# Kernel optimization log

Measured on AMD Instinct MI355X. Metric: run time of the kernel, lower is better.

The kernel has to match this reference:

```python
import jax, jax.numpy as jnp
import numpy as np

NTOKENS = 50257
NHID = 1024
TPC = int(np.ceil(np.sqrt(NTOKENS)))          # 225 tokens per class
NCLASSES = int(np.ceil(NTOKENS / TPC))        # 224 classes
BATCH = 2048
INITRANGE = 0.1


def setup_inputs() -> dict:
    key = jax.random.key(0)
    k1, k2, k3, k4 = jax.random.split(key, 4)
    inputs = jax.random.normal(k1, (BATCH, NHID), dtype=jnp.float32)
    labels = jax.random.randint(k2, (BATCH,), 0, NTOKENS, dtype=jnp.int32)
    W_top = jax.random.uniform(k3, (NHID, NCLASSES), dtype=jnp.float32,
                               minval=-INITRANGE, maxval=INITRANGE)
    b_top = jnp.zeros((NCLASSES,), dtype=jnp.float32)
    W_bottom = jax.random.uniform(k4, (NCLASSES, NHID, TPC), dtype=jnp.float32,
                                  minval=-INITRANGE, maxval=INITRANGE)
    b_bottom = jnp.zeros((NCLASSES, TPC), dtype=jnp.float32)
    return {"inputs": inputs, "labels": labels, "W_top": W_top, "b_top": b_top,
            "W_bottom": W_bottom, "b_bottom": b_bottom}


def reference(inputs, labels, W_top, b_top, W_bottom, b_bottom):
    # Two-level hierarchical softmax: P(word) = P(class | h) * P(word | class, h)
    batch = inputs.shape[0]
    cls = labels // TPC          # [B] class index at top level
    word = labels % TPC          # [B] word index within class

    # Top level: [B, nclasses]
    top_probs = jax.nn.softmax(inputs @ W_top + b_top, axis=1)
    p_cls = top_probs[jnp.arange(batch), cls]            # [B]

    # Bottom level: gather per-example class weights then batched matvec
    Wb = W_bottom[cls]                                    # [B, nhid, tpc]
    bb = b_bottom[cls]                                    # [B, tpc]
    bottom_logits = jnp.einsum('bd,bdk->bk', inputs, Wb) + bb
    bottom_probs = jax.nn.softmax(bottom_logits, axis=1)
    p_word = bottom_probs[jnp.arange(batch), word]        # [B]

    return p_cls * p_word
```

## Files before the change

kernel.cpp:

```cpp
#include <hip/hip_runtime.h>
#include <math.h>

#define TPC 225
#define NCLS 224
#define NHID 1024
#define BATCH 2048
#define CAP 256
#define LSTRIDE 256
#define NCHUNK 8
#define CHUNK_D 128
#define NDQ 32

__global__ __launch_bounds__(256) void hs_bucket(const int* __restrict__ labels,
                                                 int* __restrict__ bucket,
                                                 int* __restrict__ cnt) {
    __shared__ int scnt[NCLS];
    const int t = threadIdx.x;
    for (int i = t; i < NCLS; i += 256) scnt[i] = 0;
    __syncthreads();
    for (int b = t; b < BATCH; b += 256) {
        int lab = labels[b];
        int c = lab / TPC;
        int pos = atomicAdd(&scnt[c], 1);
        bucket[c * CAP + pos] = b;
    }
    __syncthreads();
    for (int i = t; i < NCLS; i += 256) cnt[i] = scnt[i];
}

#define LOADW(W)                                              \
    do {                                                      \
        _Pragma("unroll") for (int di = 0; di < 4; di++)      \
            _Pragma("unroll") for (int j = 0; j < 4; j++)     \
                W[di][j] = pj[j][di * KS];                    \
        _Pragma("unroll") for (int j = 0; j < 4; j++)         \
            pj[j] += 4 * KS;                                  \
    } while (0)

#define LOADX(X, dq)                                          \
    do {                                                      \
        _Pragma("unroll") for (int rl = 0; rl < RW; rl++)     \
            X[rl] = *(const float4*)(xp[rl] + (dq) * 4);      \
    } while (0)

#define FMAS(W, X)                                            \
    do {                                                      \
        _Pragma("unroll") for (int rl = 0; rl < RW; rl++) {   \
            _Pragma("unroll") for (int di = 0; di < 4; di++) {\
                float xv = ((const float*)&X[rl])[di];        \
                _Pragma("unroll") for (int j = 0; j < 4; j++) \
                    acc[rl][j] = fmaf(xv, W[di][j], acc[rl][j]); \
            }                                                 \
        }                                                     \
    } while (0)

template <int RW, int KS>
__device__ __forceinline__ void gemm_chunk(const float* __restrict__ xb,
                                           const int* rows,
                                           const float* __restrict__ wq,
                                           const int lane,
                                           float acc[RW][4]) {
    const float* xp[RW];
#pragma unroll
    for (int rl = 0; rl < RW; rl++) xp[rl] = xb + (size_t)rows[rl] * NHID;
    const float* pj[4];
#pragma unroll
    for (int j = 0; j < 4; j++) {
        int k = 64 * j + lane;
        pj[j] = wq + (k < KS ? k : KS - 1);
    }
#pragma unroll
    for (int rl = 0; rl < RW; rl++)
#pragma unroll
        for (int j = 0; j < 4; j++) acc[rl][j] = 0.f;

    float wA[4][4], wB[4][4];
    float4 xA[RW], xB[RW];
    LOADW(wA);
    LOADX(xA, 0);
    for (int dq = 0; dq < NDQ; dq += 2) {
        LOADW(wB);
        LOADX(xB, dq + 1);
        FMAS(wA, xA);
        if (dq + 2 < NDQ) {
            LOADW(wA);
            LOADX(xA, dq + 2);
        }
        FMAS(wB, xB);
    }
}

__global__ __launch_bounds__(256, 4) void hs_tlogits(const float* __restrict__ x,
                                                     const float* __restrict__ W,
                                                     float* __restrict__ twsP) {
    const int rb = blockIdx.x >> 3;
    const int q = blockIdx.x & 7;
    const int lane = threadIdx.x & 63;
    const int wr = threadIdx.x >> 6;
    int rows[2] = {rb * 8 + wr * 2, rb * 8 + wr * 2 + 1};
    const float* xb = x + q * CHUNK_D;
    const float* wq = W + (size_t)q * CHUNK_D * NCLS;
    float acc[2][4];
    gemm_chunk<2, NCLS>(xb, rows, wq, lane, acc);
    float* tp = twsP + (size_t)q * BATCH * LSTRIDE;
#pragma unroll
    for (int rl = 0; rl < 2; rl++)
#pragma unroll
        for (int j = 0; j < 4; j++) {
            int k = 64 * j + lane;
            if (k < NCLS) tp[(size_t)rows[rl] * LSTRIDE + k] = acc[rl][j];
        }
}

template <int RW>
__device__ __forceinline__ void bchunk(const float* __restrict__ xb,
                                       const float* __restrict__ wq,
                                       const int* __restrict__ bucket_c,
                                       const int base, const int n,
                                       const int lane, const int wr,
                                       float* __restrict__ bp) {
    int rows[RW], rval[RW];
#pragma unroll
    for (int rl = 0; rl < RW; rl++) {
        int idx = base + wr * RW + rl;
        rows[rl] = bucket_c[idx < n ? idx : 0];
        rval[rl] = (idx < n);
    }
    float acc[RW][4];
    gemm_chunk<RW, TPC>(xb, rows, wq, lane, acc);
#pragma unroll
    for (int rl = 0; rl < RW; rl++) {
        if (rval[rl]) {
#pragma unroll
            for (int j = 0; j < 4; j++) {
                int k = 64 * j + lane;
                if (k < TPC) bp[(size_t)rows[rl] * LSTRIDE + k] = acc[rl][j];
            }
        }
    }
}

__global__ __launch_bounds__(256, 4) void hs_blogits(const float* __restrict__ x,
                                                     const float* __restrict__ Wb,
                                                     const int* __restrict__ bucket,
                                                     const int* __restrict__ cnt,
                                                     float* __restrict__ bws) {
    const int c = blockIdx.x >> 3;
    const int q = blockIdx.x & 7;
    const int n = cnt[c];
    if (n == 0) return;
    const int lane = threadIdx.x & 63;
    const int wr = threadIdx.x >> 6;
    const float* wq = Wb + (size_t)c * (NHID * TPC) + (size_t)q * CHUNK_D * TPC;
    const float* xb = x + q * CHUNK_D;
    const int* bucket_c = bucket + c * CAP;
    float* bp = bws + (size_t)q * BATCH * LSTRIDE;

    for (int base = 0; base < n; base += 16) {
        int m = n - base;
        if (m > 16) m = 16;
        const int RW = (m + 3) >> 2;
        switch (RW) {
            case 1: bchunk<1>(xb, wq, bucket_c, base, n, lane, wr, bp); break;
            case 2: bchunk<2>(xb, wq, bucket_c, base, n, lane, wr, bp); break;
            case 3: bchunk<3>(xb, wq, bucket_c, base, n, lane, wr, bp); break;
            default: bchunk<4>(xb, wq, bucket_c, base, n, lane, wr, bp); break;
        }
    }
}

__global__ __launch_bounds__(256) void hs_finish(const float* __restrict__ tws,
                                                 const float* __restrict__ bws,
                                                 const int* __restrict__ labels,
                                                 const float* __restrict__ b_top,
                                                 const float* __restrict__ b_bot,
                                                 float* __restrict__ out) {
    const int lane = threadIdx.x & 63;
    const int wave = threadIdx.x >> 6;
    const int row = blockIdx.x * 4 + wave;
    const int label = labels[row];
    const int c = label / TPC;
    const int word = label - c * TPC;

    float p[2];
#pragma unroll
    for (int lvl = 0; lvl < 2; lvl++) {
        const int NS = lvl ? TPC : NCLS;
        const int pick = lvl ? word : c;
        const float* lws = lvl ? bws : tws;
        const float* bias = lvl ? (b_bot + c * TPC) : b_top;
        float lg[4];
#pragma unroll
        for (int j = 0; j < 4; j++) {
            int k = lane + 64 * j;
            if (k < NS) {
                float v = 0.f;
#pragma unroll
                for (int pq = 0; pq < NCHUNK; pq++)
                    v += lws[((size_t)pq * BATCH + row) * LSTRIDE + k];
                lg[j] = v + bias[k];
            } else {
                lg[j] = -INFINITY;
            }
        }
        float m = fmaxf(fmaxf(lg[0], lg[1]), fmaxf(lg[2], lg[3]));
#pragma unroll
        for (int off = 32; off > 0; off >>= 1) m = fmaxf(m, __shfl_xor(m, off, 64));
        float s = 0.f, pp = 0.f;
#pragma unroll
        for (int j = 0; j < 4; j++) {
            int k = lane + 64 * j;
            float e = (k < NS) ? __expf(lg[j] - m) : 0.f;
            s += e;
            if (k == pick) pp = e;
        }
#pragma unroll
        for (int off = 32; off > 0; off >>= 1) {
            s += __shfl_xor(s, off, 64);
            pp += __shfl_xor(pp, off, 64);
        }
        p[lvl] = pp / s;
    }
    if (lane == 0) out[row] = p[0] * p[1];
}

extern "C" void kernel_launch(void* const* d_in, const int* in_sizes, int n_in,
                              void* d_out, int out_size, void* d_ws, size_t ws_size,
                              hipStream_t stream) {
    const float* inputs   = (const float*)d_in[0];
    const int*   labels   = (const int*)d_in[1];
    const float* W_top    = (const float*)d_in[2];
    const float* b_top    = (const float*)d_in[3];
    const float* W_bottom = (const float*)d_in[4];
    const float* b_bottom = (const float*)d_in[5];
    float* out = (float*)d_out;

    int* bucket = (int*)d_ws;
    int* cnt    = bucket + NCLS * CAP;
    float* tws  = (float*)(cnt + NCLS);
    float* bws  = tws + (size_t)NCHUNK * BATCH * LSTRIDE;

    hs_bucket<<<1, 256, 0, stream>>>(labels, bucket, cnt);
    hs_tlogits<<<256 * NCHUNK, 256, 0, stream>>>(inputs, W_top, tws);
    hs_blogits<<<NCLS * NCHUNK, 256, 0, stream>>>(inputs, W_bottom, bucket, cnt, bws);
    hs_finish<<<BATCH / 4, 256, 0, stream>>>(tws, bws, labels, b_top, b_bottom, out);
}
```

Baseline: 409.9 us.

## Stage weight slabs into LDS with async double-buffered global_load_lds

Both logit GEMMs now copy 16-row weight slabs into shared memory with the direct global-to-LDS load builtin, double-buffered so the next slab loads while the current one is used. Each lane reads float4 weight vectors from LDS and owns four contiguous output columns, which allows vectorized float4 stores. The aim is to cut per-lane global weight load latency and instruction count in the inner loop. In exchange it adds a block-wide barrier per slab and LDS use that may lower occupancy, and the bottom kernel restages the weights on every 16-row pass.

```diff
diff --git a/kernel.cpp b/kernel.cpp
--- a/kernel.cpp
+++ b/kernel.cpp
@@ -1,5 +1,6 @@
 #include <hip/hip_runtime.h>
 #include <math.h>
+#include <stdint.h>
 
 #define TPC 225
 #define NCLS 224
@@ -9,7 +10,13 @@
 #define LSTRIDE 256
 #define NCHUNK 8
 #define CHUNK_D 128
-#define NDQ 32
+#define SLAB_ROWS 16
+#define NSLAB 8
+#define KSP 228
+
+typedef unsigned int u32;
+typedef __attribute__((address_space(1))) const u32 gbl_u32;
+typedef __attribute__((address_space(3))) u32 lds_u32;
 
 __global__ __launch_bounds__(256) void hs_bucket(const int* __restrict__ labels,
                                                  int* __restrict__ bucket,
@@ -28,116 +35,117 @@
     for (int i = t; i < NCLS; i += 256) cnt[i] = scnt[i];
 }
 
-#define LOADW(W)                                              \
-    do {                                                      \
-        _Pragma("unroll") for (int di = 0; di < 4; di++)      \
-            _Pragma("unroll") for (int j = 0; j < 4; j++)     \
-                W[di][j] = pj[j][di * KS];                    \
-        _Pragma("unroll") for (int j = 0; j < 4; j++)         \
-            pj[j] += 4 * KS;                                  \
-    } while (0)
-
-#define LOADX(X, dq)                                          \
-    do {                                                      \
-        _Pragma("unroll") for (int rl = 0; rl < RW; rl++)     \
-            X[rl] = *(const float4*)(xp[rl] + (dq) * 4);      \
-    } while (0)
-
-#define FMAS(W, X)                                            \
-    do {                                                      \
-        _Pragma("unroll") for (int rl = 0; rl < RW; rl++) {   \
-            _Pragma("unroll") for (int di = 0; di < 4; di++) {\
-                float xv = ((const float*)&X[rl])[di];        \
-                _Pragma("unroll") for (int j = 0; j < 4; j++) \
-                    acc[rl][j] = fmaf(xv, W[di][j], acc[rl][j]); \
-            }                                                 \
-        }                                                     \
-    } while (0)
+template <int KS>
+__device__ __forceinline__ void stage_slab(const float* __restrict__ gslab,
+                                           float* __restrict__ lbuf,
+                                           const int lane, const int wave) {
+#pragma unroll
+    for (int i = 0; i < 4; ++i) {
+        const int r = wave * 4 + i;
+        const float* gr = gslab + r * KS + lane;
+        float* lr = lbuf + r * KSP;
+#pragma unroll
+        for (int o = 0; o < 4; ++o) {
+            const int off = (o < 3) ? o * 64 : (KS - 64);
+            __builtin_amdgcn_global_load_lds((gbl_u32*)(gr + off),
+                                             (lds_u32*)(lr + off), 4, 0, 0);
+        }
+    }
+}
 
 template <int RW, int KS>
-__device__ __forceinline__ void gemm_chunk(const float* __restrict__ xb,
-                                           const int* rows,
-                                           const float* __restrict__ wq,
-                                           const int lane,
-                                           float acc[RW][4]) {
+__device__ __forceinline__ void gemm_tile_lds(const float* __restrict__ xb,
+                                              const int* rows, const int* rval,
+                                              const float* __restrict__ wtile,
+                                              float* __restrict__ lds,
+                                              float* __restrict__ outp,
+                                              const int lane, const int wave) {
     const float* xp[RW];
 #pragma unroll
     for (int rl = 0; rl < RW; rl++) xp[rl] = xb + (size_t)rows[rl] * NHID;
-    const float* pj[4];
-#pragma unroll
-    for (int j = 0; j < 4; j++) {
-        int k = 64 * j + lane;
-        pj[j] = wq + (k < KS ? k : KS - 1);
-    }
+    float acc[RW][4];
 #pragma unroll
     for (int rl = 0; rl < RW; rl++)
 #pragma unroll
         for (int j = 0; j < 4; j++) acc[rl][j] = 0.f;
 
-    float wA[4][4], wB[4][4];
-    float4 xA[RW], xB[RW];
-    LOADW(wA);
-    LOADX(xA, 0);
-    for (int dq = 0; dq < NDQ; dq += 2) {
-        LOADW(wB);
-        LOADX(xB, dq + 1);
-        FMAS(wA, xA);
-        if (dq + 2 < NDQ) {
-            LOADW(wA);
-            LOADX(xA, dq + 2);
-        }
-        FMAS(wB, xB);
+    stage_slab<KS>(wtile, lds, lane, wave);
+    __syncthreads();
+    for (int s = 0; s < NSLAB; ++s) {
+        const float* buf = lds + (s & 1) * (SLAB_ROWS * KSP);
+        if (s + 1 < NSLAB)
+            stage_slab<KS>(wtile + (s + 1) * (SLAB_ROWS * KS),
+                           lds + ((s + 1) & 1) * (SLAB_ROWS * KSP), lane, wave);
+#pragma unroll
+        for (int dql = 0; dql < 4; ++dql) {
+            const int dq = s * 4 + dql;
+            float4 xq[RW];
+#pragma unroll
+            for (int rl = 0; rl < RW; rl++)
+                xq[rl] = *(const float4*)(xp[rl] + dq * 4);
+            float4 wv[4];
+#pragma unroll
+            for (int di = 0; di < 4; di++)
+                wv[di] = *(const float4*)&buf[(dql * 4 + di) * KSP + 4 * lane];
+#pragma unroll
+            for (int rl = 0; rl < RW; rl++)
+#pragma unroll
+                for (int di = 0; di < 4; di++) {
+                    const float xv = ((const float*)&xq[rl])[di];
+                    acc[rl][0] = fmaf(xv, wv[di].x, acc[rl][0]);
+                    acc[rl][1] = fmaf(xv, wv[di].y, acc[rl][1]);
+                    acc[rl][2] = fmaf(xv, wv[di].z, acc[rl][2]);
+                    acc[rl][3] = fmaf(xv, wv[di].w, acc[rl][3]);
+                }
+        }
+        __syncthreads();
+    }
+    const int k0 = 4 * lane;
+#pragma unroll
+    for (int rl = 0; rl < RW; rl++) {
+        if (!rval[rl]) continue;
+        float* op = outp + (size_t)rows[rl] * LSTRIDE + k0;
+        if (k0 + 3 < KS) {
+            *(float4*)op = make_float4(acc[rl][0], acc[rl][1], acc[rl][2], acc[rl][3]);
+        } else {
+#pragma unroll
+            for (int j = 0; j < 4; j++)
+                if (k0 + j < KS) op[j] = acc[rl][j];
+        }
     }
 }
 
 __global__ __launch_bounds__(256, 4) void hs_tlogits(const float* __restrict__ x,
                                                      const float* __restrict__ W,
                                                      float* __restrict__ twsP) {
+    __shared__ float lds[2 * SLAB_ROWS * KSP + 32];
     const int rb = blockIdx.x >> 3;
     const int q = blockIdx.x & 7;
     const int lane = threadIdx.x & 63;
-    const int wr = threadIdx.x >> 6;
-    int rows[2] = {rb * 8 + wr * 2, rb * 8 + wr * 2 + 1};
-    const float* xb = x + q * CHUNK_D;
-    const float* wq = W + (size_t)q * CHUNK_D * NCLS;
-    float acc[2][4];
-    gemm_chunk<2, NCLS>(xb, rows, wq, lane, acc);
-    float* tp = twsP + (size_t)q * BATCH * LSTRIDE;
-#pragma unroll
-    for (int rl = 0; rl < 2; rl++)
-#pragma unroll
-        for (int j = 0; j < 4; j++) {
-            int k = 64 * j + lane;
-            if (k < NCLS) tp[(size_t)rows[rl] * LSTRIDE + k] = acc[rl][j];
-        }
+    const int wave = threadIdx.x >> 6;
+    int rows[2] = {rb * 8 + wave * 2, rb * 8 + wave * 2 + 1};
+    int rval[2] = {1, 1};
+    const float* wtile = W + (size_t)q * CHUNK_D * NCLS;
+    gemm_tile_lds<2, NCLS>(x + q * CHUNK_D, rows, rval, wtile, lds,
+                           twsP + (size_t)q * BATCH * LSTRIDE, lane, wave);
 }
 
 template <int RW>
-__device__ __forceinline__ void bchunk(const float* __restrict__ xb,
-                                       const float* __restrict__ wq,
-                                       const int* __restrict__ bucket_c,
-                                       const int base, const int n,
-                                       const int lane, const int wr,
-                                       float* __restrict__ bp) {
+__device__ __forceinline__ void bpass_lds(const float* __restrict__ xb,
+                                          const float* __restrict__ wtile,
+                                          const int* __restrict__ bucket_c,
+                                          const int base, const int n,
+                                          float* __restrict__ lds,
+                                          float* __restrict__ bp,
+                                          const int lane, const int wave) {
     int rows[RW], rval[RW];
 #pragma unroll
     for (int rl = 0; rl < RW; rl++) {
-        int idx = base + wr * RW + rl;
+        int idx = base + wave * RW + rl;
         rows[rl] = bucket_c[idx < n ? idx : 0];
         rval[rl] = (idx < n);
     }
-    float acc[RW][4];
-    gemm_chunk<RW, TPC>(xb, rows, wq, lane, acc);
-#pragma unroll
-    for (int rl = 0; rl < RW; rl++) {
-        if (rval[rl]) {
-#pragma unroll
-            for (int j = 0; j < 4; j++) {
-                int k = 64 * j + lane;
-                if (k < TPC) bp[(size_t)rows[rl] * LSTRIDE + k] = acc[rl][j];
-            }
-        }
-    }
+    gemm_tile_lds<RW, TPC>(xb, rows, rval, wtile, lds, bp, lane, wave);
 }
 
 __global__ __launch_bounds__(256, 4) void hs_blogits(const float* __restrict__ x,
@@ -145,13 +153,14 @@
                                                      const int* __restrict__ bucket,
                                                      const int* __restrict__ cnt,
                                                      float* __restrict__ bws) {
+    __shared__ float lds[2 * SLAB_ROWS * KSP + 32];
     const int c = blockIdx.x >> 3;
     const int q = blockIdx.x & 7;
     const int n = cnt[c];
     if (n == 0) return;
     const int lane = threadIdx.x & 63;
-    const int wr = threadIdx.x >> 6;
-    const float* wq = Wb + (size_t)c * (NHID * TPC) + (size_t)q * CHUNK_D * TPC;
+    const int wave = threadIdx.x >> 6;
+    const float* wtile = Wb + (size_t)c * (NHID * TPC) + (size_t)q * CHUNK_D * TPC;
     const float* xb = x + q * CHUNK_D;
     const int* bucket_c = bucket + c * CAP;
     float* bp = bws + (size_t)q * BATCH * LSTRIDE;
@@ -161,10 +170,10 @@
         if (m > 16) m = 16;
         const int RW = (m + 3) >> 2;
         switch (RW) {
-            case 1: bchunk<1>(xb, wq, bucket_c, base, n, lane, wr, bp); break;
-            case 2: bchunk<2>(xb, wq, bucket_c, base, n, lane, wr, bp); break;
-            case 3: bchunk<3>(xb, wq, bucket_c, base, n, lane, wr, bp); break;
-            default: bchunk<4>(xb, wq, bucket_c, base, n, lane, wr, bp); break;
+            case 1: bpass_lds<1>(xb, wtile, bucket_c, base, n, lds, bp, lane, wave); break;
+            case 2: bpass_lds<2>(xb, wtile, bucket_c, base, n, lds, bp, lane, wave); break;
+            case 3: bpass_lds<3>(xb, wtile, bucket_c, base, n, lds, bp, lane, wave); break;
+            default: bpass_lds<4>(xb, wtile, bucket_c, base, n, lds, bp, lane, wave); break;
         }
     }
 }
```

Result: slower. 1.444 ms (+252.2%).
